# Kernel tuning notes

Measured on AMD Instinct MI355X. Metric: run time of the kernel, lower is better.

The kernel has to match this reference:

```python
import jax, jax.numpy as jnp
import numpy as np

N_NODES = 100000
N_EDGES = 1000000
NODE_DIM = 128
EDGE_DIM = 16
HID = 128


def _linear_init(key, fan_in, fan_out):
    # torch nn.Linear default: U(-1/sqrt(fan_in), 1/sqrt(fan_in))
    kw, kb = jax.random.split(key)
    bound = 1.0 / np.sqrt(fan_in)
    W = jax.random.uniform(kw, (fan_in, fan_out), jnp.float32, -bound, bound)
    b = jax.random.uniform(kb, (fan_out,), jnp.float32, -bound, bound)
    return W, b


def setup_inputs() -> dict:
    key = jax.random.key(0)
    ks = jax.random.split(key, 12)
    node_features = jax.random.normal(ks[0], (N_NODES, NODE_DIM), jnp.float32)
    edge_index = jax.random.randint(ks[1], (2, N_EDGES), 0, N_NODES, jnp.int64 if jax.config.read('jax_enable_x64') else jnp.int32)
    edge_features = jax.random.normal(ks[2], (N_EDGES, EDGE_DIM), jnp.float32)
    Wn1, bn1 = _linear_init(ks[3], NODE_DIM, HID)
    Wn2, bn2 = _linear_init(ks[4], HID, HID)
    We1, be1 = _linear_init(ks[5], EDGE_DIM, HID)
    We2, be2 = _linear_init(ks[6], HID, HID)
    Wp1, bp1 = _linear_init(ks[7], HID * 3, HID)
    Wp2, bp2 = _linear_init(ks[8], HID, HID // 2)
    Wp3, bp3 = _linear_init(ks[9], HID // 2, 1)
    return dict(node_features=node_features, edge_index=edge_index, edge_features=edge_features,
                Wn1=Wn1, bn1=bn1, Wn2=Wn2, bn2=bn2,
                We1=We1, be1=be1, We2=We2, be2=be2,
                Wp1=Wp1, bp1=bp1, Wp2=Wp2, bp2=bp2, Wp3=Wp3, bp3=bp3)


def reference(node_features, edge_index, edge_features,
              Wn1, bn1, Wn2, bn2, We1, be1, We2, be2,
              Wp1, bp1, Wp2, bp2, Wp3, bp3):
    # node/edge encoders: Linear -> ReLU -> Linear
    node_emb = jax.nn.relu(node_features @ Wn1 + bn1) @ Wn2 + bn2  # [N, H]
    edge_emb = jax.nn.relu(edge_features @ We1 + be1) @ We2 + be2  # [E, H]
    src = node_emb[edge_index[0]]  # [E, H] gather
    dst = node_emb[edge_index[1]]  # [E, H] gather
    combined = jnp.concatenate([src, dst, edge_emb], axis=1)  # [E, 3H]
    # predictor MLP (Dropout(0.2) is identity at inference)
    h = jax.nn.relu(combined @ Wp1 + bp1)
    h = jax.nn.relu(h @ Wp2 + bp2)
    scores = jax.nn.sigmoid(h @ Wp3 + bp3)  # [E, 1]
    return scores
```

## Files before the change

### kernel.cpp

```cpp
#include <hip/hip_runtime.h>

typedef _Float16 f16;
typedef _Float16 f16x8 __attribute__((ext_vector_type(8)));
typedef float    f32x4 __attribute__((ext_vector_type(4)));
typedef f16x8 f16x8_a __attribute__((may_alias));
typedef f16   f16_a   __attribute__((may_alias));

#define NN 100000
#define NE 1000000

static __device__ __forceinline__ f32x4 mfma16(f16x8 a, f16x8 b, f32x4 c) {
  return __builtin_amdgcn_mfma_f32_16x16x32_f16(a, b, c, 0, 0, 0);
}

static __device__ __forceinline__ f16x8 zero8() {
  f16x8 z; 
#pragma unroll
  for (int j = 0; j < 8; ++j) z[j] = (f16)0.f;
  return z;
}

template<int RB_LOG2, int SZ>
static __device__ __forceinline__ void load_weights(const f16* __restrict__ gw, char* lds) {
  const char* src = (const char*)gw;
#pragma unroll
  for (int g = threadIdx.x; g < SZ / 16; g += 256) {
    int byte = g << 4;
    int row  = byte >> RB_LOG2;
    int dstb = byte ^ ((row & 7) << 4);
    f16x8 v = *(const f16x8_a*)(src + byte);
    *(f16x8_a*)(lds + dstb) = v;
  }
}

template<int RB_LOG2>
static __device__ __forceinline__ f16x8 read_b(const char* lds, int n, int kbyte) {
  int byte = ((n << RB_LOG2) + kbyte) ^ ((n & 7) << 4);
  return *(const f16x8_a*)(lds + byte);
}

static __device__ __forceinline__ f16x8 act_read(const char* act, int base, int m, int kbyte) {
  int byte = (base + m * 256 + kbyte) ^ ((m & 7) << 4);
  return *(const f16x8_a*)(act + byte);
}

static __device__ __forceinline__ void act_write(char* act, int base, int m, int col, f16 v) {
  int byte = (base + m * 256 + col * 2) ^ ((m & 7) << 4);
  *(f16_a*)(act + byte) = v;
}

__global__ void transpose_w(const float* __restrict__ src, f16* __restrict__ dst,
                            int K, int N, int kOff, int ld) {
  int i = blockIdx.x * 256 + threadIdx.x;
  if (i >= N * K) return;
  int n = i / K, k = i - n * K;
  dst[i] = (f16)src[(size_t)(kOff + k) * ld + n];
}

__global__ __launch_bounds__(256, 2) void node_kernel(
    const float* __restrict__ nf, const f16* __restrict__ WnT1, const float* __restrict__ bn1,
    const f16* __restrict__ WnT2, const float* __restrict__ bn2, f16* __restrict__ emb) {
  __shared__ char wbuf[32768];
  __shared__ char act[32768];
  const int tid = threadIdx.x, w = tid >> 6, lane = tid & 63;
  const int c = lane & 15, kb = lane >> 4;
  const int base = blockIdx.x * 128 + w * 32;
  const int abase = w * 8192;

  load_weights<8, 32768>(WnT1, wbuf);
  __syncthreads();

  f16x8 a[2][4];
#pragma unroll
  for (int rt = 0; rt < 2; ++rt) {
    int r = base + rt * 16 + c; r = r < NN ? r : 0;
    const float* p = nf + (size_t)r * 128 + kb * 8;
#pragma unroll
    for (int ks = 0; ks < 4; ++ks) {
      float4 x0 = *(const float4*)(p + ks * 32);
      float4 x1 = *(const float4*)(p + ks * 32 + 4);
      f16x8 t;
      t[0]=(f16)x0.x; t[1]=(f16)x0.y; t[2]=(f16)x0.z; t[3]=(f16)x0.w;
      t[4]=(f16)x1.x; t[5]=(f16)x1.y; t[6]=(f16)x1.z; t[7]=(f16)x1.w;
      a[rt][ks] = t;
    }
  }

  f32x4 acc[2][8];
#pragma unroll
  for (int nt = 0; nt < 8; ++nt) {
    float bb = bn1[nt * 16 + c];
    acc[0][nt] = f32x4{bb, bb, bb, bb};
    acc[1][nt] = f32x4{bb, bb, bb, bb};
  }
#pragma unroll
  for (int ks = 0; ks < 4; ++ks)
#pragma unroll
    for (int nt = 0; nt < 8; ++nt) {
      f16x8 b = read_b<8>(wbuf, nt * 16 + c, ks * 64 + kb * 16);
      acc[0][nt] = mfma16(a[0][ks], b, acc[0][nt]);
      acc[1][nt] = mfma16(a[1][ks], b, acc[1][nt]);
    }
#pragma unroll
  for (int rt = 0; rt < 2; ++rt)
#pragma unroll
    for (int nt = 0; nt < 8; ++nt)
#pragma unroll
      for (int r = 0; r < 4; ++r) {
        float v = acc[rt][nt][r];
        v = v > 0.f ? v : 0.f;
        act_write(act, abase, rt * 16 + kb * 4 + r, nt * 16 + c, (f16)v);
      }

  __syncthreads();
  load_weights<8, 32768>(WnT2, wbuf);
  __syncthreads();

  f32x4 acc2[2][8];
#pragma unroll
  for (int nt = 0; nt < 8; ++nt) {
    float bb = bn2[nt * 16 + c];
    acc2[0][nt] = f32x4{bb, bb, bb, bb};
    acc2[1][nt] = f32x4{bb, bb, bb, bb};
  }
#pragma unroll
  for (int ks = 0; ks < 4; ++ks) {
    f16x8 a0 = act_read(act, abase, c,      ks * 64 + kb * 16);
    f16x8 a1 = act_read(act, abase, 16 + c, ks * 64 + kb * 16);
#pragma unroll
    for (int nt = 0; nt < 8; ++nt) {
      f16x8 b = read_b<8>(wbuf, nt * 16 + c, ks * 64 + kb * 16);
      acc2[0][nt] = mfma16(a0, b, acc2[0][nt]);
      acc2[1][nt] = mfma16(a1, b, acc2[1][nt]);
    }
  }
#pragma unroll
  for (int rt = 0; rt < 2; ++rt)
#pragma unroll
    for (int nt = 0; nt < 8; ++nt)
#pragma unroll
      for (int r = 0; r < 4; ++r) {
        int row = base + rt * 16 + kb * 4 + r;
        if (row < NN) emb[(size_t)row * 128 + nt * 16 + c] = (f16)acc2[rt][nt][r];
      }
}

__global__ __launch_bounds__(256, 2) void edge_kernel(
    const float* __restrict__ ef, const int* __restrict__ eidx,
    const f16* __restrict__ emb,
    const f16* __restrict__ WeT1, const float* __restrict__ be1,
    const f16* __restrict__ WeT2, const float* __restrict__ be2,
    const f16* __restrict__ Wp1a, const f16* __restrict__ Wp1b, const f16* __restrict__ Wp1c,
    const float* __restrict__ bp1,
    const f16* __restrict__ WpT2, const float* __restrict__ bp2,
    const float* __restrict__ Wp3, const float* __restrict__ bp3,
    float* __restrict__ out) {
  __shared__ char wbuf[32768];
  __shared__ char act[32768];
  const int tid = threadIdx.x, w = tid >> 6, lane = tid & 63;
  const int c = lane & 15, kb = lane >> 4;
  const int ebase = blockIdx.x * 128 + w * 32;
  const int abase = w * 8192;

  load_weights<5, 4096>(WeT1, wbuf);
  __syncthreads();
  {
    f16x8 a[2];
#pragma unroll
    for (int rt = 0; rt < 2; ++rt) {
      int m = ebase + rt * 16 + c; m = m < NE ? m : 0;
      f16x8 t = zero8();
      if (kb < 2) {
        const float* p = ef + (size_t)m * 16 + kb * 8;
        float4 x0 = *(const float4*)(p);
        float4 x1 = *(const float4*)(p + 4);
        t[0]=(f16)x0.x; t[1]=(f16)x0.y; t[2]=(f16)x0.z; t[3]=(f16)x0.w;
        t[4]=(f16)x1.x; t[5]=(f16)x1.y; t[6]=(f16)x1.z; t[7]=(f16)x1.w;
      }
      a[rt] = t;
    }
    f32x4 acc[2][8];
#pragma unroll
    for (int nt = 0; nt < 8; ++nt) {
      float bb = be1[nt * 16 + c];
      acc[0][nt] = f32x4{bb, bb, bb, bb};
      acc[1][nt] = f32x4{bb, bb, bb, bb};
    }
    int kbyte = (kb < 2) ? kb * 16 : 0;
#pragma unroll
    for (int nt = 0; nt < 8; ++nt) {
      f16x8 b = read_b<5>(wbuf, nt * 16 + c, kbyte);
      acc[0][nt] = mfma16(a[0], b, acc[0][nt]);
      acc[1][nt] = mfma16(a[1], b, acc[1][nt]);
    }
#pragma unroll
    for (int rt = 0; rt < 2; ++rt)
#pragma unroll
      for (int nt = 0; nt < 8; ++nt)
#pragma unroll
        for (int r = 0; r < 4; ++r) {
          float v = acc[rt][nt][r];
          v = v > 0.f ? v : 0.f;
          act_write(act, abase, rt * 16 + kb * 4 + r, nt * 16 + c, (f16)v);
        }
  }

  __syncthreads();
  load_weights<8, 32768>(WeT2, wbuf);
  __syncthreads();
  {
    f32x4 acc[2][8];
#pragma unroll
    for (int nt = 0; nt < 8; ++nt) {
      float bb = be2[nt * 16 + c];
      acc[0][nt] = f32x4{bb, bb, bb, bb};
      acc[1][nt] = f32x4{bb, bb, bb, bb};
    }
#pragma unroll
    for (int ks = 0; ks < 4; ++ks) {
      f16x8 a0 = act_read(act, abase, c,      ks * 64 + kb * 16);
      f16x8 a1 = act_read(act, abase, 16 + c, ks * 64 + kb * 16);
#pragma unroll
      for (int nt = 0; nt < 8; ++nt) {
        f16x8 b = read_b<8>(wbuf, nt * 16 + c, ks * 64 + kb * 16);
        acc[0][nt] = mfma16(a0, b, acc[0][nt]);
        acc[1][nt] = mfma16(a1, b, acc[1][nt]);
      }
    }
#pragma unroll
    for (int rt = 0; rt < 2; ++rt)
#pragma unroll
      for (int nt = 0; nt < 8; ++nt)
#pragma unroll
        for (int r = 0; r < 4; ++r)
          act_write(act, abase, rt * 16 + kb * 4 + r, nt * 16 + c, (f16)acc[rt][nt][r]);
  }

  f32x4 accp[2][8];
#pragma unroll
  for (int nt = 0; nt < 8; ++nt) {
    float bb = bp1[nt * 16 + c];
    accp[0][nt] = f32x4{bb, bb, bb, bb};
    accp[1][nt] = f32x4{bb, bb, bb, bb};
  }

  __syncthreads();
  load_weights<8, 32768>(Wp1a, wbuf);
  __syncthreads();
  {
    f16x8 a[2][4];
#pragma unroll
    for (int rt = 0; rt < 2; ++rt) {
      int m = ebase + rt * 16 + c; m = m < NE ? m : NE - 1;
      int s = eidx[m];
      const f16* np = emb + (size_t)s * 128 + kb * 8;
#pragma unroll
      for (int ks = 0; ks < 4; ++ks) a[rt][ks] = *(const f16x8_a*)(np + ks * 32);
    }
#pragma unroll
    for (int ks = 0; ks < 4; ++ks)
#pragma unroll
      for (int nt = 0; nt < 8; ++nt) {
        f16x8 b = read_b<8>(wbuf, nt * 16 + c, ks * 64 + kb * 16);
        accp[0][nt] = mfma16(a[0][ks], b, accp[0][nt]);
        accp[1][nt] = mfma16(a[1][ks], b, accp[1][nt]);
      }
  }

  __syncthreads();
  load_weights<8, 32768>(Wp1b, wbuf);
  __syncthreads();
  {
    f16x8 a[2][4];
#pragma unroll
    for (int rt = 0; rt < 2; ++rt) {
      int m = ebase + rt * 16 + c; m = m < NE ? m : NE - 1;
      int s = eidx[NE + m];
      const f16* np = emb + (size_t)s * 128 + kb * 8;
#pragma unroll
      for (int ks = 0; ks < 4; ++ks) a[rt][ks] = *(const f16x8_a*)(np + ks * 32);
    }
#pragma unroll
    for (int ks = 0; ks < 4; ++ks)
#pragma unroll
      for (int nt = 0; nt < 8; ++nt) {
        f16x8 b = read_b<8>(wbuf, nt * 16 + c, ks * 64 + kb * 16);
        accp[0][nt] = mfma16(a[0][ks], b, accp[0][nt]);
        accp[1][nt] = mfma16(a[1][ks], b, accp[1][nt]);
      }
  }

  __syncthreads();
  load_weights<8, 32768>(Wp1c, wbuf);
  __syncthreads();
  {
#pragma unroll
    for (int ks = 0; ks < 4; ++ks) {
      f16x8 a0 = act_read(act, abase, c,      ks * 64 + kb * 16);
      f16x8 a1 = act_read(act, abase, 16 + c, ks * 64 + kb * 16);
#pragma unroll
      for (int nt = 0; nt < 8; ++nt) {
        f16x8 b = read_b<8>(wbuf, nt * 16 + c, ks * 64 + kb * 16);
        accp[0][nt] = mfma16(a0, b, accp[0][nt]);
        accp[1][nt] = mfma16(a1, b, accp[1][nt]);
      }
    }
#pragma unroll
    for (int rt = 0; rt < 2; ++rt)
#pragma unroll
      for (int nt = 0; nt < 8; ++nt)
#pragma unroll
        for (int r = 0; r < 4; ++r) {
          float v = accp[rt][nt][r];
          v = v > 0.f ? v : 0.f;
          act_write(act, abase, rt * 16 + kb * 4 + r, nt * 16 + c, (f16)v);
        }
  }

  __syncthreads();
  load_weights<8, 16384>(WpT2, wbuf);
  __syncthreads();
  f32x4 accq[2][4];
#pragma unroll
  for (int nt = 0; nt < 4; ++nt) {
    float bb = bp2[nt * 16 + c];
    accq[0][nt] = f32x4{bb, bb, bb, bb};
    accq[1][nt] = f32x4{bb, bb, bb, bb};
  }
#pragma unroll
  for (int ks = 0; ks < 4; ++ks) {
    f16x8 a0 = act_read(act, abase, c,      ks * 64 + kb * 16);
    f16x8 a1 = act_read(act, abase, 16 + c, ks * 64 + kb * 16);
#pragma unroll
    for (int nt = 0; nt < 4; ++nt) {
      f16x8 b = read_b<8>(wbuf, nt * 16 + c, ks * 64 + kb * 16);
      accq[0][nt] = mfma16(a0, b, accq[0][nt]);
      accq[1][nt] = mfma16(a1, b, accq[1][nt]);
    }
  }

  float w3[4], b3 = bp3[0];
#pragma unroll
  for (int nt = 0; nt < 4; ++nt) w3[nt] = Wp3[nt * 16 + c];
#pragma unroll
  for (int rt = 0; rt < 2; ++rt) {
#pragma unroll
    for (int r = 0; r < 4; ++r) {
      float s = 0.f;
#pragma unroll
      for (int nt = 0; nt < 4; ++nt) {
        float h = accq[rt][nt][r];
        h = h > 0.f ? h : 0.f;
        s += h * w3[nt];
      }
      s += __shfl_xor(s, 1, 64);
      s += __shfl_xor(s, 2, 64);
      s += __shfl_xor(s, 4, 64);
      s += __shfl_xor(s, 8, 64);
      int m = ebase + rt * 16 + kb * 4 + r;
      if (c == r && m < NE) {
        out[m] = 1.f / (1.f + __expf(-(s + b3)));
      }
    }
  }
}

extern "C" void kernel_launch(void* const* d_in, const int* in_sizes, int n_in,
                              void* d_out, int out_size, void* d_ws, size_t ws_size,
                              hipStream_t stream) {
  const float* nf  = (const float*)d_in[0];
  const int*   ei  = (const int*)  d_in[1];
  const float* ef  = (const float*)d_in[2];
  const float* Wn1 = (const float*)d_in[3];
  const float* bn1 = (const float*)d_in[4];
  const float* Wn2 = (const float*)d_in[5];
  const float* bn2 = (const float*)d_in[6];
  const float* We1 = (const float*)d_in[7];
  const float* be1 = (const float*)d_in[8];
  const float* We2 = (const float*)d_in[9];
  const float* be2 = (const float*)d_in[10];
  const float* Wp1 = (const float*)d_in[11];
  const float* bp1 = (const float*)d_in[12];
  const float* Wp2 = (const float*)d_in[13];
  const float* bp2 = (const float*)d_in[14];
  const float* Wp3 = (const float*)d_in[15];
  const float* bp3 = (const float*)d_in[16];

  char* ws = (char*)d_ws;
  f16* WnT1 = (f16*)(ws);
  f16* WnT2 = (f16*)(ws + 32768);
  f16* WeT1 = (f16*)(ws + 65536);
  f16* WeT2 = (f16*)(ws + 69632);
  f16* Wp1a = (f16*)(ws + 102400);
  f16* Wp1b = (f16*)(ws + 135168);
  f16* Wp1c = (f16*)(ws + 167936);
  f16* WpT2 = (f16*)(ws + 200704);
  f16* emb  = (f16*)(ws + 217088);

  transpose_w<<<64, 256, 0, stream>>>(Wn1, WnT1, 128, 128, 0, 128);
  transpose_w<<<64, 256, 0, stream>>>(Wn2, WnT2, 128, 128, 0, 128);
  transpose_w<<<8,  256, 0, stream>>>(We1, WeT1, 16,  128, 0, 128);
  transpose_w<<<64, 256, 0, stream>>>(We2, WeT2, 128, 128, 0, 128);
  transpose_w<<<64, 256, 0, stream>>>(Wp1, Wp1a, 128, 128, 0,   128);
  transpose_w<<<64, 256, 0, stream>>>(Wp1, Wp1b, 128, 128, 128, 128);
  transpose_w<<<64, 256, 0, stream>>>(Wp1, Wp1c, 128, 128, 256, 128);
  transpose_w<<<32, 256, 0, stream>>>(Wp2, WpT2, 128, 64, 0, 64);

  node_kernel<<<782, 256, 0, stream>>>(nf, WnT1, bn1, WnT2, bn2, emb);
  edge_kernel<<<7813, 256, 0, stream>>>(ef, ei, emb, WeT1, be1, WeT2, be2,
                                        Wp1a, Wp1b, Wp1c, bp1, WpT2, bp2, Wp3, bp3,
                                        (float*)d_out);
}
```

Before: 485.1 us.

## Fold edge encoder second layer into predictor, persistent pipelined edge kernel

Precomputes We2·Wp1c and a folded bias so the edge encoder's second linear layer merges into the predictor's first layer, removing one 128x128 GEMM per edge. The edge kernel becomes persistent with 256 blocks. Each block keeps all predictor weights resident in LDS, which removes the per-block weight reloads and barriers. Each wave double-buffers the next tile's indices, edge features and gathered embeddings in registers to overlap loads with MFMA work. Weight-prep launches are merged into two kernels and nontemporal loads and stores are added. The risks are register pressure at 1 block per CU, a 144KB LDS footprint, and fp16 rounding of the folded weight product.

```diff
diff --git a/kernel.cpp b/kernel.cpp
--- a/kernel.cpp
+++ b/kernel.cpp
@@ -3,21 +3,33 @@
 typedef _Float16 f16;
 typedef _Float16 f16x8 __attribute__((ext_vector_type(8)));
 typedef float    f32x4 __attribute__((ext_vector_type(4)));
+typedef float    fv4   __attribute__((ext_vector_type(4)));
 typedef f16x8 f16x8_a __attribute__((may_alias));
 typedef f16   f16_a   __attribute__((may_alias));
+typedef fv4   fv4_a   __attribute__((may_alias));
 
 #define NN 100000
 #define NE 1000000
+#define NT_TILES 31250
+#define EK_BLOCKS 256
+#define NW (EK_BLOCKS * 4)
 
 static __device__ __forceinline__ f32x4 mfma16(f16x8 a, f16x8 b, f32x4 c) {
   return __builtin_amdgcn_mfma_f32_16x16x32_f16(a, b, c, 0, 0, 0);
 }
 
 static __device__ __forceinline__ f16x8 zero8() {
-  f16x8 z; 
+  f16x8 z;
 #pragma unroll
   for (int j = 0; j < 8; ++j) z[j] = (f16)0.f;
   return z;
+}
+
+static __device__ __forceinline__ f16x8 cvt8(fv4 x0, fv4 x1) {
+  f16x8 t;
+  t[0]=(f16)x0[0]; t[1]=(f16)x0[1]; t[2]=(f16)x0[2]; t[3]=(f16)x0[3];
+  t[4]=(f16)x1[0]; t[5]=(f16)x1[1]; t[6]=(f16)x1[2]; t[7]=(f16)x1[3];
+  return t;
 }
 
 template<int RB_LOG2, int SZ>
@@ -49,12 +61,40 @@
   *(f16_a*)(act + byte) = v;
 }
 
-__global__ void transpose_w(const float* __restrict__ src, f16* __restrict__ dst,
-                            int K, int N, int kOff, int ld) {
-  int i = blockIdx.x * 256 + threadIdx.x;
-  if (i >= N * K) return;
-  int n = i / K, k = i - n * K;
-  dst[i] = (f16)src[(size_t)(kOff + k) * ld + n];
+__global__ void prep_transpose(const float* __restrict__ Wn1, const float* __restrict__ Wn2,
+                               const float* __restrict__ We1, const float* __restrict__ Wp1,
+                               const float* __restrict__ Wp2,
+                               f16* __restrict__ WnT1, f16* __restrict__ WnT2,
+                               f16* __restrict__ WeT1, f16* __restrict__ WaT,
+                               f16* __restrict__ WbT,  f16* __restrict__ WpT2) {
+  int b = blockIdx.x, t = threadIdx.x;
+  if (b < 64)       { int i = b * 256 + t;        int n = i >> 7, k = i & 127; WnT1[i] = (f16)Wn1[(size_t)k * 128 + n]; }
+  else if (b < 128) { int i = (b - 64) * 256 + t; int n = i >> 7, k = i & 127; WnT2[i] = (f16)Wn2[(size_t)k * 128 + n]; }
+  else if (b < 136) { int i = (b - 128) * 256 + t; int n = i >> 4, k = i & 15; WeT1[i] = (f16)We1[(size_t)k * 128 + n]; }
+  else if (b < 200) { int i = (b - 136) * 256 + t; int n = i >> 7, k = i & 127; WaT[i] = (f16)Wp1[(size_t)k * 128 + n]; }
+  else if (b < 264) { int i = (b - 200) * 256 + t; int n = i >> 7, k = i & 127; WbT[i] = (f16)Wp1[(size_t)(128 + k) * 128 + n]; }
+  else              { int i = (b - 264) * 256 + t; int n = i >> 7, k = i & 127; WpT2[i] = (f16)Wp2[(size_t)k * 64 + n]; }
+}
+
+__global__ void prep_fold(const float* __restrict__ We2, const float* __restrict__ Wp1,
+                          const float* __restrict__ bp1, const float* __restrict__ be2,
+                          f16* __restrict__ WCT, float* __restrict__ bfold) {
+  int b = blockIdx.x, t = threadIdx.x;
+  if (b < 64) {
+    int i = b * 256 + t;
+    int n = i >> 7, k = i & 127;
+    float s = 0.f;
+#pragma unroll 8
+    for (int m = 0; m < 128; ++m)
+      s += We2[(size_t)k * 128 + m] * Wp1[(size_t)(256 + m) * 128 + n];
+    WCT[i] = (f16)s;
+  } else if (t < 128) {
+    float s = bp1[t];
+#pragma unroll 8
+    for (int m = 0; m < 128; ++m)
+      s += be2[m] * Wp1[(size_t)(256 + m) * 128 + t];
+    bfold[t] = s;
+  }
 }
 
 __global__ __launch_bounds__(256, 2) void node_kernel(
@@ -70,129 +110,34 @@
   load_weights<8, 32768>(WnT1, wbuf);
   __syncthreads();
 
-  f16x8 a[2][4];
-#pragma unroll
-  for (int rt = 0; rt < 2; ++rt) {
-    int r = base + rt * 16 + c; r = r < NN ? r : 0;
-    const float* p = nf + (size_t)r * 128 + kb * 8;
-#pragma unroll
-    for (int ks = 0; ks < 4; ++ks) {
-      float4 x0 = *(const float4*)(p + ks * 32);
-      float4 x1 = *(const float4*)(p + ks * 32 + 4);
-      f16x8 t;
-      t[0]=(f16)x0.x; t[1]=(f16)x0.y; t[2]=(f16)x0.z; t[3]=(f16)x0.w;
-      t[4]=(f16)x1.x; t[5]=(f16)x1.y; t[6]=(f16)x1.z; t[7]=(f16)x1.w;
-      a[rt][ks] = t;
-    }
-  }
-
-  f32x4 acc[2][8];
-#pragma unroll
-  for (int nt = 0; nt < 8; ++nt) {
-    float bb = bn1[nt * 16 + c];
-    acc[0][nt] = f32x4{bb, bb, bb, bb};
-    acc[1][nt] = f32x4{bb, bb, bb, bb};
-  }
-#pragma unroll
-  for (int ks = 0; ks < 4; ++ks)
+  {
+    f16x8 a[2][4];
+#pragma unroll
+    for (int rt = 0; rt < 2; ++rt) {
+      int r = base + rt * 16 + c; r = r < NN ? r : 0;
+      const fv4* p = (const fv4*)(nf + (size_t)r * 128 + kb * 8);
+#pragma unroll
+      for (int ks = 0; ks < 4; ++ks) {
+        fv4 x0 = __builtin_nontemporal_load(p + ks * 8);
+        fv4 x1 = __builtin_nontemporal_load(p + ks * 8 + 1);
+        a[rt][ks] = cvt8(x0, x1);
+      }
+    }
+    f32x4 acc[2][8];
 #pragma unroll
     for (int nt = 0; nt < 8; ++nt) {
-      f16x8 b = read_b<8>(wbuf, nt * 16 + c, ks * 64 + kb * 16);
-      acc[0][nt] = mfma16(a[0][ks], b, acc[0][nt]);
-      acc[1][nt] = mfma16(a[1][ks], b, acc[1][nt]);
-    }
-#pragma unroll
-  for (int rt = 0; rt < 2; ++rt)
-#pragma unroll
-    for (int nt = 0; nt < 8; ++nt)
-#pragma unroll
-      for (int r = 0; r < 4; ++r) {
-        float v = acc[rt][nt][r];
-        v = v > 0.f ? v : 0.f;
-        act_write(act, abase, rt * 16 + kb * 4 + r, nt * 16 + c, (f16)v);
-      }
-
-  __syncthreads();
-  load_weights<8, 32768>(WnT2, wbuf);
-  __syncthreads();
-
-  f32x4 acc2[2][8];
-#pragma unroll
-  for (int nt = 0; nt < 8; ++nt) {
-    float bb = bn2[nt * 16 + c];
-    acc2[0][nt] = f32x4{bb, bb, bb, bb};
-    acc2[1][nt] = f32x4{bb, bb, bb, bb};
-  }
-#pragma unroll
-  for (int ks = 0; ks < 4; ++ks) {
-    f16x8 a0 = act_read(act, abase, c,      ks * 64 + kb * 16);
-    f16x8 a1 = act_read(act, abase, 16 + c, ks * 64 + kb * 16);
-#pragma unroll
-    for (int nt = 0; nt < 8; ++nt) {
-      f16x8 b = read_b<8>(wbuf, nt * 16 + c, ks * 64 + kb * 16);
-      acc2[0][nt] = mfma16(a0, b, acc2[0][nt]);
-      acc2[1][nt] = mfma16(a1, b, acc2[1][nt]);
-    }
-  }
-#pragma unroll
-  for (int rt = 0; rt < 2; ++rt)
-#pragma unroll
-    for (int nt = 0; nt < 8; ++nt)
-#pragma unroll
-      for (int r = 0; r < 4; ++r) {
-        int row = base + rt * 16 + kb * 4 + r;
-        if (row < NN) emb[(size_t)row * 128 + nt * 16 + c] = (f16)acc2[rt][nt][r];
-      }
-}
-
-__global__ __launch_bounds__(256, 2) void edge_kernel(
-    const float* __restrict__ ef, const int* __restrict__ eidx,
-    const f16* __restrict__ emb,
-    const f16* __restrict__ WeT1, const float* __restrict__ be1,
-    const f16* __restrict__ WeT2, const float* __restrict__ be2,
-    const f16* __restrict__ Wp1a, const f16* __restrict__ Wp1b, const f16* __restrict__ Wp1c,
-    const float* __restrict__ bp1,
-    const f16* __restrict__ WpT2, const float* __restrict__ bp2,
-    const float* __restrict__ Wp3, const float* __restrict__ bp3,
-    float* __restrict__ out) {
-  __shared__ char wbuf[32768];
-  __shared__ char act[32768];
-  const int tid = threadIdx.x, w = tid >> 6, lane = tid & 63;
-  const int c = lane & 15, kb = lane >> 4;
-  const int ebase = blockIdx.x * 128 + w * 32;
-  const int abase = w * 8192;
-
-  load_weights<5, 4096>(WeT1, wbuf);
-  __syncthreads();
-  {
-    f16x8 a[2];
-#pragma unroll
-    for (int rt = 0; rt < 2; ++rt) {
-      int m = ebase + rt * 16 + c; m = m < NE ? m : 0;
-      f16x8 t = zero8();
-      if (kb < 2) {
-        const float* p = ef + (size_t)m * 16 + kb * 8;
-        float4 x0 = *(const float4*)(p);
-        float4 x1 = *(const float4*)(p + 4);
-        t[0]=(f16)x0.x; t[1]=(f16)x0.y; t[2]=(f16)x0.z; t[3]=(f16)x0.w;
-        t[4]=(f16)x1.x; t[5]=(f16)x1.y; t[6]=(f16)x1.z; t[7]=(f16)x1.w;
-      }
-      a[rt] = t;
-    }
-    f32x4 acc[2][8];
-#pragma unroll
-    for (int nt = 0; nt < 8; ++nt) {
-      float bb = be1[nt * 16 + c];
+      float bb = bn1[nt * 16 + c];
       acc[0][nt] = f32x4{bb, bb, bb, bb};
       acc[1][nt] = f32x4{bb, bb, bb, bb};
     }
-    int kbyte = (kb < 2) ? kb * 16 : 0;
-#pragma unroll
-    for (int nt = 0; nt < 8; ++nt) {
-      f16x8 b = read_b<5>(wbuf, nt * 16 + c, kbyte);
-      acc[0][nt] = mfma16(a[0], b, acc[0][nt]);
-      acc[1][nt] = mfma16(a[1], b, acc[1][nt]);
-    }
+#pragma unroll
+    for (int ks = 0; ks < 4; ++ks)
+#pragma unroll
+      for (int nt = 0; nt < 8; ++nt) {
+        f16x8 b = read_b<8>(wbuf, nt * 16 + c, ks * 64 + kb * 16);
+        acc[0][nt] = mfma16(a[0][ks], b, acc[0][nt]);
+        acc[1][nt] = mfma16(a[1][ks], b, acc[1][nt]);
+      }
 #pragma unroll
     for (int rt = 0; rt < 2; ++rt)
 #pragma unroll
@@ -206,13 +151,14 @@
   }
 
   __syncthreads();
-  load_weights<8, 32768>(WeT2, wbuf);
+  load_weights<8, 32768>(WnT2, wbuf);
   __syncthreads();
+
   {
     f32x4 acc[2][8];
 #pragma unroll
     for (int nt = 0; nt < 8; ++nt) {
-      float bb = be2[nt * 16 + c];
+      float bb = bn2[nt * 16 + c];
       acc[0][nt] = f32x4{bb, bb, bb, bb};
       acc[1][nt] = f32x4{bb, bb, bb, bb};
     }
@@ -232,79 +178,152 @@
 #pragma unroll
       for (int nt = 0; nt < 8; ++nt)
 #pragma unroll
-        for (int r = 0; r < 4; ++r)
-          act_write(act, abase, rt * 16 + kb * 4 + r, nt * 16 + c, (f16)acc[rt][nt][r]);
-  }
-
-  f32x4 accp[2][8];
+        for (int r = 0; r < 4; ++r) {
+          int row = base + rt * 16 + kb * 4 + r;
+          if (row < NN) emb[(size_t)row * 128 + nt * 16 + c] = (f16)acc[rt][nt][r];
+        }
+  }
+}
+
+struct Tile {
+  int s0, s1, d0, d1;
+  fv4 e00, e01, e10, e11;
+  f16x8 ga0[4], ga1[4], gb0[4], gb1[4];
+};
+
+__global__ __launch_bounds__(256, 1) void edge_kernel(
+    const float* __restrict__ ef, const int* __restrict__ eidx,
+    const f16* __restrict__ WeT1, const float* __restrict__ be1,
+    const f16* __restrict__ WaT, const f16* __restrict__ WbT,
+    const f16* __restrict__ WCT, const f16* __restrict__ WpT2g,
+    const float* __restrict__ bfold, const float* __restrict__ bp2,
+    const float* __restrict__ Wp3, const float* __restrict__ bp3,
+    const f16* __restrict__ emb, float* __restrict__ out) {
+  __shared__ char wa[32768];
+  __shared__ char wb[32768];
+  __shared__ char wc[32768];
+  __shared__ char wp2l[16384];
+  __shared__ char act[32768];
+  const int tid = threadIdx.x, w = tid >> 6, lane = tid & 63;
+  const int c = lane & 15, kb = lane >> 4;
+  const int abase = w * 8192;
+
+  load_weights<8, 32768>(WaT, wa);
+  load_weights<8, 32768>(WbT, wb);
+  load_weights<8, 32768>(WCT, wc);
+  load_weights<8, 16384>(WpT2g, wp2l);
+  __syncthreads();
+
+  f16x8 w1frag[8];
+  float bias_e1[8], bias_p1[8], bias_p2[4], w3[4];
 #pragma unroll
   for (int nt = 0; nt < 8; ++nt) {
-    float bb = bp1[nt * 16 + c];
-    accp[0][nt] = f32x4{bb, bb, bb, bb};
-    accp[1][nt] = f32x4{bb, bb, bb, bb};
-  }
-
-  __syncthreads();
-  load_weights<8, 32768>(Wp1a, wbuf);
-  __syncthreads();
-  {
-    f16x8 a[2][4];
-#pragma unroll
-    for (int rt = 0; rt < 2; ++rt) {
-      int m = ebase + rt * 16 + c; m = m < NE ? m : NE - 1;
-      int s = eidx[m];
-      const f16* np = emb + (size_t)s * 128 + kb * 8;
-#pragma unroll
-      for (int ks = 0; ks < 4; ++ks) a[rt][ks] = *(const f16x8_a*)(np + ks * 32);
-    }
-#pragma unroll
-    for (int ks = 0; ks < 4; ++ks)
-#pragma unroll
-      for (int nt = 0; nt < 8; ++nt) {
-        f16x8 b = read_b<8>(wbuf, nt * 16 + c, ks * 64 + kb * 16);
-        accp[0][nt] = mfma16(a[0][ks], b, accp[0][nt]);
-        accp[1][nt] = mfma16(a[1][ks], b, accp[1][nt]);
-      }
-  }
-
-  __syncthreads();
-  load_weights<8, 32768>(Wp1b, wbuf);
-  __syncthreads();
-  {
-    f16x8 a[2][4];
-#pragma unroll
-    for (int rt = 0; rt < 2; ++rt) {
-      int m = ebase + rt * 16 + c; m = m < NE ? m : NE - 1;
-      int s = eidx[NE + m];
-      const f16* np = emb + (size_t)s * 128 + kb * 8;
-#pragma unroll
-      for (int ks = 0; ks < 4; ++ks) a[rt][ks] = *(const f16x8_a*)(np + ks * 32);
-    }
-#pragma unroll
-    for (int ks = 0; ks < 4; ++ks)
-#pragma unroll
-      for (int nt = 0; nt < 8; ++nt) {
-        f16x8 b = read_b<8>(wbuf, nt * 16 + c, ks * 64 + kb * 16);
-        accp[0][nt] = mfma16(a[0][ks], b, accp[0][nt]);
-        accp[1][nt] = mfma16(a[1][ks], b, accp[1][nt]);
-      }
-  }
-
-  __syncthreads();
-  load_weights<8, 32768>(Wp1c, wbuf);
-  __syncthreads();
-  {
+    w1frag[nt] = *(const f16x8_a*)(WeT1 + (nt * 16 + c) * 16 + (kb & 1) * 8);
+    bias_e1[nt] = be1[nt * 16 + c];
+    bias_p1[nt] = bfold[nt * 16 + c];
+  }
+#pragma unroll
+  for (int nt = 0; nt < 4; ++nt) { bias_p2[nt] = bp2[nt * 16 + c]; w3[nt] = Wp3[nt * 16 + c]; }
+  const float b3 = bp3[0];
+
+  auto LOAD_IDX = [&](int t, Tile& T) {
+    int e0 = t * 32 + c;
+    T.s0 = __builtin_nontemporal_load(eidx + e0);
+    T.s1 = __builtin_nontemporal_load(eidx + e0 + 16);
+    T.d0 = __builtin_nontemporal_load(eidx + NE + e0);
+    T.d1 = __builtin_nontemporal_load(eidx + NE + e0 + 16);
+  };
+  auto LOAD_EF = [&](int t, Tile& T) {
+    if (kb < 2) {
+      const fv4* p = (const fv4*)(ef + (size_t)(t * 32 + c) * 16 + kb * 8);
+      T.e00 = __builtin_nontemporal_load(p);
+      T.e01 = __builtin_nontemporal_load(p + 1);
+      const fv4* q = (const fv4*)(ef + (size_t)(t * 32 + 16 + c) * 16 + kb * 8);
+      T.e10 = __builtin_nontemporal_load(q);
+      T.e11 = __builtin_nontemporal_load(q + 1);
+    }
+  };
+  auto LOAD_G = [&](Tile& T) {
+    const f16* p0 = emb + (size_t)T.s0 * 128 + kb * 8;
+    const f16* p1 = emb + (size_t)T.s1 * 128 + kb * 8;
+    const f16* q0 = emb + (size_t)T.d0 * 128 + kb * 8;
+    const f16* q1 = emb + (size_t)T.d1 * 128 + kb * 8;
+#pragma unroll
+    for (int ks = 0; ks < 4; ++ks) {
+      T.ga0[ks] = *(const f16x8_a*)(p0 + ks * 32);
+      T.ga1[ks] = *(const f16x8_a*)(p1 + ks * 32);
+      T.gb0[ks] = *(const f16x8_a*)(q0 + ks * 32);
+      T.gb1[ks] = *(const f16x8_a*)(q1 + ks * 32);
+    }
+  };
+
+  auto BODY = [&](int t, Tile& C0, Tile& N0, int pft) {
+    LOAD_IDX(pft, N0);
+    LOAD_EF(pft, N0);
+
+    {
+      f16x8 ae0 = zero8(), ae1 = zero8();
+      if (kb < 2) { ae0 = cvt8(C0.e00, C0.e01); ae1 = cvt8(C0.e10, C0.e11); }
+      f32x4 acc1[2][8];
+#pragma unroll
+      for (int nt = 0; nt < 8; ++nt) {
+        acc1[0][nt] = f32x4{bias_e1[nt], bias_e1[nt], bias_e1[nt], bias_e1[nt]};
+        acc1[1][nt] = acc1[0][nt];
+      }
+#pragma unroll
+      for (int nt = 0; nt < 8; ++nt) {
+        acc1[0][nt] = mfma16(ae0, w1frag[nt], acc1[0][nt]);
+        acc1[1][nt] = mfma16(ae1, w1frag[nt], acc1[1][nt]);
+      }
+#pragma unroll
+      for (int rt = 0; rt < 2; ++rt)
+#pragma unroll
+        for (int nt = 0; nt < 8; ++nt)
+#pragma unroll
+          for (int r = 0; r < 4; ++r) {
+            float v = acc1[rt][nt][r];
+            v = v > 0.f ? v : 0.f;
+            act_write(act, abase, rt * 16 + kb * 4 + r, nt * 16 + c, (f16)v);
+          }
+    }
+
+    f32x4 accp[2][8];
+#pragma unroll
+    for (int nt = 0; nt < 8; ++nt) {
+      accp[0][nt] = f32x4{bias_p1[nt], bias_p1[nt], bias_p1[nt], bias_p1[nt]};
+      accp[1][nt] = accp[0][nt];
+    }
 #pragma unroll
     for (int ks = 0; ks < 4; ++ks) {
       f16x8 a0 = act_read(act, abase, c,      ks * 64 + kb * 16);
       f16x8 a1 = act_read(act, abase, 16 + c, ks * 64 + kb * 16);
 #pragma unroll
       for (int nt = 0; nt < 8; ++nt) {
-        f16x8 b = read_b<8>(wbuf, nt * 16 + c, ks * 64 + kb * 16);
+        f16x8 b = read_b<8>(wc, nt * 16 + c, ks * 64 + kb * 16);
         accp[0][nt] = mfma16(a0, b, accp[0][nt]);
         accp[1][nt] = mfma16(a1, b, accp[1][nt]);
       }
     }
+
+    LOAD_G(N0);
+
+#pragma unroll
+    for (int ks = 0; ks < 4; ++ks)
+#pragma unroll
+      for (int nt = 0; nt < 8; ++nt) {
+        f16x8 b = read_b<8>(wa, nt * 16 + c, ks * 64 + kb * 16);
+        accp[0][nt] = mfma16(C0.ga0[ks], b, accp[0][nt]);
+        accp[1][nt] = mfma16(C0.ga1[ks], b, accp[1][nt]);
+      }
+#pragma unroll
+    for (int ks = 0; ks < 4; ++ks)
+#pragma unroll
+      for (int nt = 0; nt < 8; ++nt) {
+        f16x8 b = read_b<8>(wb, nt * 16 + c, ks * 64 + kb * 16);
+        accp[0][nt] = mfma16(C0.gb0[ks], b, accp[0][nt]);
+        accp[1][nt] = mfma16(C0.gb1[ks], b, accp[1][nt]);
+      }
+
 #pragma unroll
     for (int rt = 0; rt < 2; ++rt)
 #pragma unroll
@@ -315,52 +334,61 @@
           v = v > 0.f ? v : 0.f;
           act_write(act, abase, rt * 16 + kb * 4 + r, nt * 16 + c, (f16)v);
         }
-  }
-
-  __syncthreads();
-  load_weights<8, 16384>(WpT2, wbuf);
-  __syncthreads();
-  f32x4 accq[2][4];
-#pragma unroll
-  for (int nt = 0; nt < 4; ++nt) {
-    float bb = bp2[nt * 16 + c];
-    accq[0][nt] = f32x4{bb, bb, bb, bb};
-    accq[1][nt] = f32x4{bb, bb, bb, bb};
-  }
-#pragma unroll
-  for (int ks = 0; ks < 4; ++ks) {
-    f16x8 a0 = act_read(act, abase, c,      ks * 64 + kb * 16);
-    f16x8 a1 = act_read(act, abase, 16 + c, ks * 64 + kb * 16);
+
+    f32x4 accq[2][4];
 #pragma unroll
     for (int nt = 0; nt < 4; ++nt) {
-      f16x8 b = read_b<8>(wbuf, nt * 16 + c, ks * 64 + kb * 16);
-      accq[0][nt] = mfma16(a0, b, accq[0][nt]);
-      accq[1][nt] = mfma16(a1, b, accq[1][nt]);
-    }
-  }
-
-  float w3[4], b3 = bp3[0];
-#pragma unroll
-  for (int nt = 0; nt < 4; ++nt) w3[nt] = Wp3[nt * 16 + c];
-#pragma unroll
-  for (int rt = 0; rt < 2; ++rt) {
-#pragma unroll
-    for (int r = 0; r < 4; ++r) {
-      float s = 0.f;
+      accq[0][nt] = f32x4{bias_p2[nt], bias_p2[nt], bias_p2[nt], bias_p2[nt]};
+      accq[1][nt] = accq[0][nt];
+    }
+#pragma unroll
+    for (int ks = 0; ks < 4; ++ks) {
+      f16x8 a0 = act_read(act, abase, c,      ks * 64 + kb * 16);
+      f16x8 a1 = act_read(act, abase, 16 + c, ks * 64 + kb * 16);
 #pragma unroll
       for (int nt = 0; nt < 4; ++nt) {
-        float h = accq[rt][nt][r];
-        h = h > 0.f ? h : 0.f;
-        s += h * w3[nt];
-      }
-      s += __shfl_xor(s, 1, 64);
-      s += __shfl_xor(s, 2, 64);
-      s += __shfl_xor(s, 4, 64);
-      s += __shfl_xor(s, 8, 64);
-      int m = ebase + rt * 16 + kb * 4 + r;
-      if (c == r && m < NE) {
-        out[m] = 1.f / (1.f + __expf(-(s + b3)));
-      }
+        f16x8 b = read_b<8>(wp2l, nt * 16 + c, ks * 64 + kb * 16);
+        accq[0][nt] = mfma16(a0, b, accq[0][nt]);
+        accq[1][nt] = mfma16(a1, b, accq[1][nt]);
+      }
+    }
+
+#pragma unroll
+    for (int rt = 0; rt < 2; ++rt) {
+#pragma unroll
+      for (int r = 0; r < 4; ++r) {
+        float s = 0.f;
+#pragma unroll
+        for (int nt = 0; nt < 4; ++nt) {
+          float h = accq[rt][nt][r];
+          h = h > 0.f ? h : 0.f;
+          s += h * w3[nt];
+        }
+        s += __shfl_xor(s, 1, 64);
+        s += __shfl_xor(s, 2, 64);
+        s += __shfl_xor(s, 4, 64);
+        s += __shfl_xor(s, 8, 64);
+        if (c == r) {
+          int m = t * 32 + rt * 16 + kb * 4 + r;
+          float v = 1.f / (1.f + __expf(-(s + b3)));
+          __builtin_nontemporal_store(v, out + m);
+        }
+      }
+    }
+  };
+
+  const int gw = blockIdx.x * 4 + w;
+  Tile A, B;
+  LOAD_IDX(gw, A);
+  LOAD_EF(gw, A);
+  LOAD_G(A);
+
+  for (int t = gw; t < NT_TILES; t += 2 * NW) {
+    int t1 = t + NW;
+    BODY(t, A, B, t1 < NT_TILES ? t1 : t);
+    if (t1 < NT_TILES) {
+      int t2 = t1 + NW;
+      BODY(t1, B, A, t2 < NT_TILES ? t2 : t1);
     }
   }
 }
@@ -387,27 +415,20 @@
   const float* bp3 = (const float*)d_in[16];
 
   char* ws = (char*)d_ws;
-  f16* WnT1 = (f16*)(ws);
-  f16* WnT2 = (f16*)(ws + 32768);
-  f16* WeT1 = (f16*)(ws + 65536);
-  f16* WeT2 = (f16*)(ws + 69632);
-  f16* Wp1a = (f16*)(ws + 102400);
-  f16* Wp1b = (f16*)(ws + 135168);
-  f16* Wp1c = (f16*)(ws + 167936);
-  f16* WpT2 = (f16*)(ws + 200704);
-  f16* emb  = (f16*)(ws + 217088);
-
-  transpose_w<<<64, 256, 0, stream>>>(Wn1, WnT1, 128, 128, 0, 128);
-  transpose_w<<<64, 256, 0, stream>>>(Wn2, WnT2, 128, 128, 0, 128);
-  transpose_w<<<8,  256, 0, stream>>>(We1, WeT1, 16,  128, 0, 128);
-  transpose_w<<<64, 256, 0, stream>>>(We2, WeT2, 128, 128, 0, 128);
-  transpose_w<<<64, 256, 0, stream>>>(Wp1, Wp1a, 128, 128, 0,   128);
-  transpose_w<<<64, 256, 0, stream>>>(Wp1, Wp1b, 128, 128, 128, 128);
-  transpose_w<<<64, 256, 0, stream>>>(Wp1, Wp1c, 128, 128, 256, 128);
-  transpose_w<<<32, 256, 0, stream>>>(Wp2, WpT2, 128, 64, 0, 64);
-
+  f16*   WnT1  = (f16*)(ws);
+  f16*   WnT2  = (f16*)(ws + 32768);
+  f16*   WeT1  = (f16*)(ws + 65536);
+  f16*   WaT   = (f16*)(ws + 69632);
+  f16*   WbT   = (f16*)(ws + 102400);
+  f16*   WCT   = (f16*)(ws + 135168);
+  f16*   WpT2  = (f16*)(ws + 167936);
+  float* bfold = (float*)(ws + 184320);
+  f16*   emb   = (f16*)(ws + 184832);
+
+  prep_transpose<<<296, 256, 0, stream>>>(Wn1, Wn2, We1, Wp1, Wp2,
+                                          WnT1, WnT2, WeT1, WaT, WbT, WpT2);
+  prep_fold<<<65, 256, 0, stream>>>(We2, Wp1, bp1, be2, WCT, bfold);
   node_kernel<<<782, 256, 0, stream>>>(nf, WnT1, bn1, WnT2, bn2, emb);
-  edge_kernel<<<7813, 256, 0, stream>>>(ef, ei, emb, WeT1, be1, WeT2, be2,
-                                        Wp1a, Wp1b, Wp1c, bp1, WpT2, bp2, Wp3, bp3,
-                                        (float*)d_out);
-}
+  edge_kernel<<<EK_BLOCKS, 256, 0, stream>>>(ef, ei, WeT1, be1, WaT, WbT, WCT, WpT2,
+                                             bfold, bp2, Wp3, bp3, emb, (float*)d_out);
+}
```

After: 476.9 us. About the same (-1.7%).
